# Optimization experiments

Measured on AMD Instinct MI355X. Metric: run time of the kernel, lower is better.

The kernel has to match this reference:

```python
import jax, jax.numpy as jnp
import numpy as np

N_NODES = 100000
N_EDGES = 1600000
NUM_FEATURES = 128
DIMS = [(NUM_FEATURES, 50), (50, 50), (50, 30), (30, 30), (30, 10), (10, 10), (10, 1)]


def setup_inputs() -> dict:
    key = jax.random.key(0)
    ks = jax.random.split(key, 4 + 2 * len(DIMS))
    inp = {
        "x": jax.random.normal(ks[0], (N_NODES, NUM_FEATURES), dtype=jnp.float32),
        "edge_index": jax.random.randint(ks[1], (2, N_EDGES), 0, N_NODES, dtype=jnp.int64) if jax.config.read("jax_enable_x64") else jax.random.randint(ks[1], (2, N_EDGES), 0, N_NODES, dtype=jnp.int32),
        "edge_weight": jax.random.uniform(ks[2], (N_EDGES,), dtype=jnp.float32),
    }
    for i, (fi, fo) in enumerate(DIMS):
        scale = 1.0 / np.sqrt(fi)
        inp[f"W{i+1}"] = jax.random.normal(ks[3 + 2 * i], (fi, fo), dtype=jnp.float32) * scale
        inp[f"b{i+1}"] = jax.random.normal(ks[4 + 2 * i], (fo,), dtype=jnp.float32) * 0.01
    return inp


def _gcn_norm(edge_index, edge_weight, n):
    # Add self-loops with weight 1, then symmetric normalization (PyG GCNConv).
    loops = jnp.arange(n)
    row = jnp.concatenate([edge_index[0], loops])
    col = jnp.concatenate([edge_index[1], loops])
    w = jnp.concatenate([edge_weight, jnp.ones((n,), edge_weight.dtype)])
    deg = jnp.zeros((n,), edge_weight.dtype).at[col].add(w)
    dinv = jnp.where(deg > 0, 1.0 / jnp.sqrt(deg), 0.0)
    norm = dinv[row] * w * dinv[col]
    return row, col, norm


def _gcn_conv(x, row, col, norm, W, b):
    h = x @ W                                # [N, out]
    msg = h[row] * norm[:, None]             # gather + edge scale [E+N, out]
    out = jnp.zeros_like(h).at[col].add(msg) # scatter-add
    return out + b


def _forward(x, edge_index, edge_weight, params):
    n = x.shape[0]
    row, col, norm = _gcn_norm(edge_index, edge_weight, n)  # shared across layers
    h = x
    n_layers = len(params)
    for i, (W, b) in enumerate(params):
        h = _gcn_conv(h, row, col, norm, W, b)
        if i < n_layers - 1:
            h = jax.nn.relu(h)
        # F.dropout treated as identity (eval mode) for a deterministic reference
    return h


def reference(x, edge_index, edge_weight, W1, b1, W2, b2, W3, b3, W4, b4, W5, b5, W6, b6, W7, b7):
    params = [(W1, b1), (W2, b2), (W3, b3), (W4, b4), (W5, b5), (W6, b6), (W7, b7)]
    return _forward(x, edge_index, edge_weight, params)
```

## Files before the change

### kernel.cpp

```cpp
#include <hip/hip_runtime.h>
#include <hip/hip_fp16.h>


static constexpr int NN = 100000;
static constexpr int NE = 1600000;
static constexpr int BKL = 9;
static constexpr int NBUK = (NN + 511) >> BKL;
static constexpr int EPT = 8;
static constexpr int EB = (NE + 2047) / 2048;


__global__ __launch_bounds__(256) void k_hist0(const int* __restrict__ col,
                                               int* __restrict__ counts) {
    __shared__ int lh[NBUK];
    for (int j = threadIdx.x; j < NBUK; j += 256) lh[j] = 0;
    __syncthreads();
    int base = blockIdx.x * 2048;
#pragma unroll
    for (int k = 0; k < EPT; ++k) {
        int e = base + k * 256 + threadIdx.x;
        if (e < NE) atomicAdd(&lh[col[e] >> BKL], 1);
    }
    __syncthreads();
    for (int j = threadIdx.x; j < NBUK; j += 256)
        counts[j * EB + blockIdx.x] = lh[j];
}


__global__ __launch_bounds__(256) void k_scanA(int* __restrict__ counts,
                                               int* __restrict__ btot) {
    __shared__ int lds[256];
    const int b = blockIdx.x;
    const int t = threadIdx.x;
    int* c = counts + (size_t)b * EB;
    constexpr int PER = (EB + 255) / 256;
    int v[PER];
    int s = 0;
#pragma unroll
    for (int k = 0; k < PER; ++k) {
        int idx = t * PER + k;
        v[k] = (idx < EB) ? c[idx] : 0;
        s += v[k];
    }
    lds[t] = s;
    __syncthreads();
    for (int off = 1; off < 256; off <<= 1) {
        int u = (t >= off) ? lds[t - off] : 0;
        __syncthreads();
        lds[t] += u;
        __syncthreads();
    }
    int run = lds[t] - s;
#pragma unroll
    for (int k = 0; k < PER; ++k) {
        int idx = t * PER + k;
        if (idx < EB) { c[idx] = run; run += v[k]; }
    }
    if (t == 255) btot[b] = lds[255];
}


__global__ void k_scanB(const int* __restrict__ btot, int* __restrict__ bstart) {
    __shared__ int lds[256];
    int t = threadIdx.x;
    int v = (t < NBUK) ? btot[t] : 0;
    lds[t] = v;
    __syncthreads();
    for (int off = 1; off < 256; off <<= 1) {
        int u = (t >= off) ? lds[t - off] : 0;
        __syncthreads();
        lds[t] += u;
        __syncthreads();
    }
    if (t < NBUK) bstart[t] = lds[t] - v;
    if (t == 0) bstart[NBUK] = NE;
}


__global__ __launch_bounds__(256) void k_A1(const int* __restrict__ row,
                                            const int* __restrict__ col,
                                            const float* __restrict__ ew,
                                            const int* __restrict__ counts,
                                            const int* __restrict__ bstart,
                                            int2* __restrict__ stg) {
    __shared__ int cur[NBUK];
    for (int j = threadIdx.x; j < NBUK; j += 256)
        cur[j] = bstart[j] + counts[j * EB + blockIdx.x];
    __syncthreads();
    int base = blockIdx.x * 2048;
#pragma unroll
    for (int k = 0; k < EPT; ++k) {
        int e = base + k * 256 + threadIdx.x;
        if (e < NE) {
            int c = col[e], r = row[e];
            int pos = atomicAdd(&cur[c >> BKL], 1);
            stg[pos] = make_int2(((c & 511) << 17) | r, __float_as_int(ew[e]));
        }
    }
}


__global__ __launch_bounds__(256) void k_bdeg(const int* __restrict__ bstart,
                                              const int2* __restrict__ stg,
                                              float* __restrict__ dinv) {
    __shared__ float sdeg[512];
    const int b = blockIdx.x;
    for (int j = threadIdx.x; j < 512; j += 256) sdeg[j] = 0.0f;
    __syncthreads();
    const int s = bstart[b], e = bstart[b + 1];
    for (int p = s + threadIdx.x; p < e; p += 256) {
        int2 rec = stg[p];
        atomicAdd(&sdeg[rec.x >> 17], __int_as_float(rec.y));
    }
    __syncthreads();
    for (int j = threadIdx.x; j < 512; j += 256) {
        int idx = (b << BKL) + j;
        if (idx < NN) dinv[idx] = rsqrtf(sdeg[j] + 1.0f);
    }
}


__global__ __launch_bounds__(512) void k_place(const int* __restrict__ bstart,
                                               const int2* __restrict__ stg,
                                               const float* __restrict__ dinv,
                                               int* __restrict__ offs,
                                               int2* __restrict__ csw) {
    __shared__ int lcnt[512];
    __shared__ int cur[512];
    const int b = blockIdx.x;
    const int t = threadIdx.x;
    lcnt[t] = 0;
    __syncthreads();
    const int s = bstart[b], e = bstart[b + 1];
    for (int p = s + t; p < e; p += 512)
        atomicAdd(&lcnt[stg[p].x >> 17], 1);
    __syncthreads();
    int v = lcnt[t];
    for (int off = 1; off < 512; off <<= 1) {
        int u = (t >= off) ? lcnt[t - off] : 0;
        __syncthreads();
        lcnt[t] += u;
        __syncthreads();
    }
    int excl = lcnt[t] - v;
    int idx = (b << BKL) + t;
    if (idx <= NN) offs[idx] = s + excl;
    cur[t] = s + excl;
    __syncthreads();
    for (int p = s + t; p < e; p += 512) {
        int2 rec = stg[p];
        int cl = rec.x >> 17;
        int r = rec.x & 0x1FFFF;
        float nw = dinv[r] * __int_as_float(rec.y) * dinv[(b << BKL) + cl];
        int slot = atomicAdd(&cur[cl], 1);
        csw[slot] = make_int2(r, __float_as_int(nw));
    }
}


template <int FIN, int FOUT, int S, int NSPL>
__global__ __launch_bounds__(256, 2) void k_matmul_f(const float* __restrict__ X,
                                                     const float* __restrict__ W,
                                                     __half* __restrict__ H) {
    constexpr int FC = FOUT / NSPL;
    constexpr int NG = FIN / 16;
    const int node = (blockIdx.x >> 1) * 256 + threadIdx.x;
    const int ch = blockIdx.x & 1;
    if (node >= NN) return;
    const float* xr = X + (size_t)node * FIN;
    float acc[FC];
#pragma unroll
    for (int j = 0; j < FC; ++j) acc[j] = 0.0f;

    float4 buf[2][4];
#pragma unroll
    for (int g = 0; g < 4; ++g) buf[0][g] = *(const float4*)(xr + 4 * g);
#pragma unroll
    for (int grp = 0; grp < NG; ++grp) {
        const int cur = grp & 1;
        if (grp + 1 < NG) {
#pragma unroll
            for (int g = 0; g < 4; ++g)
                buf[cur ^ 1][g] = *(const float4*)(xr + (grp + 1) * 16 + 4 * g);
        }
#pragma unroll
        for (int g = 0; g < 4; ++g)
#pragma unroll
            for (int kk = 0; kk < 4; ++kk) {
                float xv = ((const float*)&buf[cur][g])[kk];
                const float* wrow = W + (grp * 16 + 4 * g + kk) * FOUT + ch * FC;
#pragma unroll
                for (int j = 0; j < FC; ++j) acc[j] = fmaf(xv, wrow[j], acc[j]);
            }
    }
    __half* hr = H + (size_t)node * S + ch * FC;
#pragma unroll
    for (int j = 0; j < FC; ++j) hr[j] = __float2half_rn(acc[j]);
}


template <int FIN, int SX, int FOUT, int S, int NSPL>
__global__ __launch_bounds__(256, 2) void k_matmul_h(const __half* __restrict__ X,
                                                     const float* __restrict__ W,
                                                     __half* __restrict__ H) {
    constexpr int FC = FOUT / NSPL;
    constexpr int NCH = (FIN + 7) / 8;
    const int node = blockIdx.x * 256 + threadIdx.x;
    const int ch = blockIdx.y;
    if (node >= NN) return;
    const __half* xr = X + (size_t)node * SX;
    int4 raw[NCH];
#pragma unroll
    for (int c = 0; c < NCH; ++c) raw[c] = *(const int4*)(xr + 8 * c);
    float acc[FC];
#pragma unroll
    for (int j = 0; j < FC; ++j) acc[j] = 0.0f;
#pragma unroll
    for (int c = 0; c < NCH; ++c) {
        const __half2* hp = (const __half2*)&raw[c];
        const int lim = (FIN - 8 * c < 8) ? FIN - 8 * c : 8;
#pragma unroll
        for (int kk = 0; kk < 8; ++kk) {
            if (kk < lim) {
                __half2 pair = hp[kk >> 1];
                float xv = (kk & 1) ? __high2float(pair) : __low2float(pair);
                const float* wrow = W + (8 * c + kk) * FOUT + ch * FC;
#pragma unroll
                for (int j = 0; j < FC; ++j) acc[j] = fmaf(xv, wrow[j], acc[j]);
            }
        }
    }
    __half* hr = H + (size_t)node * S + ch * FC;
#pragma unroll
    for (int j = 0; j < FC; ++j) hr[j] = __float2half_rn(acc[j]);
}

__global__ void k_matmul_1h(const __half* __restrict__ X, const float* __restrict__ W,
                            float* __restrict__ H) {
    int i = blockIdx.x * blockDim.x + threadIdx.x;
    if (i >= NN) return;
    const __half* xr = X + (size_t)i * 16;
    int4 r0 = *(const int4*)xr;
    __half2 r1 = *(const __half2*)(xr + 8);
    const __half2* hp = (const __half2*)&r0;
    float acc = 0.0f;
#pragma unroll
    for (int q = 0; q < 4; ++q) {
        acc = fmaf(__low2float(hp[q]), W[2 * q], acc);
        acc = fmaf(__high2float(hp[q]), W[2 * q + 1], acc);
    }
    acc = fmaf(__low2float(r1), W[8], acc);
    acc = fmaf(__high2float(r1), W[9], acc);
    H[i] = acc;
}


static __device__ __forceinline__ int2 nt_load2(const int2* p) {
    unsigned long long raw = __builtin_nontemporal_load((const unsigned long long*)p);
    return make_int2((int)(raw & 0xFFFFFFFFull), (int)(raw >> 32));
}

template <int F, int SH, int SA, int LPN, bool RELU>
__global__ __launch_bounds__(256) void k_agg2(const int* __restrict__ offs,
                                              const int2* __restrict__ csw,
                                              const __half2* __restrict__ H,
                                              const float* __restrict__ dinv,
                                              const float* __restrict__ b,
                                              __half* __restrict__ O) {
    constexpr int R = F / 2;
    int t = blockIdx.x * blockDim.x + threadIdx.x;
    int g = t / LPN;
    int f = t - g * LPN;
    if (g >= NN) return;
    const int q0 = 4 * f;
    if (q0 >= R) return;
    int p = offs[g];
    const int pe = offs[g + 1];
    const int pl = pe - 1;

    float2 acc[4];
#pragma unroll
    for (int c = 0; c < 4; ++c) acc[c] = make_float2(0.f, 0.f);

    for (; p < pe; p += 4) {
        int2 e[4];
#pragma unroll
        for (int i = 0; i < 4; ++i) e[i] = nt_load2(csw + min(p + i, pl));
        __half2 h[4][4];
#pragma unroll
        for (int i = 0; i < 4; ++i)
            *(int4*)h[i] = *(const int4*)(H + (size_t)e[i].x * SH + q0);
#pragma unroll
        for (int i = 0; i < 4; ++i) {
            float w = (p + i < pe) ? __int_as_float(e[i].y) : 0.0f;
#pragma unroll
            for (int c = 0; c < 4; ++c) {
                acc[c].x = fmaf(__low2float(h[i][c]), w, acc[c].x);
                acc[c].y = fmaf(__high2float(h[i][c]), w, acc[c].y);
            }
        }
    }

    float di = dinv[g];
    float d2 = di * di;
    __half2 hs[4];
    *(int4*)hs = *(const int4*)(H + (size_t)g * SH + q0);
    __half2* orow = (__half2*)(O + (size_t)g * SA) + q0;
#pragma unroll
    for (int c = 0; c < 4; ++c) {
        if (q0 + c < R) {
            float vx = acc[c].x + fmaf(__low2float(hs[c]), d2, b[2 * (q0 + c)]);
            float vy = acc[c].y + fmaf(__high2float(hs[c]), d2, b[2 * (q0 + c) + 1]);
            if (RELU) { vx = fmaxf(vx, 0.f); vy = fmaxf(vy, 0.f); }
            orow[c] = __floats2half2_rn(vx, vy);
        }
    }
}

__global__ void k_agg1(const int* __restrict__ offs, const int2* __restrict__ csw,
                       const float* __restrict__ H, const float* __restrict__ dinv,
                       const float* __restrict__ b, float* __restrict__ O) {
    int g = blockIdx.x * blockDim.x + threadIdx.x;
    if (g >= NN) return;
    int p = offs[g];
    const int pe = offs[g + 1];
    const int pl = pe - 1;
    float a0 = 0.f, a1 = 0.f, a2 = 0.f, a3 = 0.f;
    for (; p < pe; p += 4) {
        int2 e0 = nt_load2(csw + min(p, pl)),     e1 = nt_load2(csw + min(p + 1, pl));
        int2 e2 = nt_load2(csw + min(p + 2, pl)), e3 = nt_load2(csw + min(p + 3, pl));
        float w0 = (p < pe)     ? __int_as_float(e0.y) : 0.f;
        float w1 = (p + 1 < pe) ? __int_as_float(e1.y) : 0.f;
        float w2 = (p + 2 < pe) ? __int_as_float(e2.y) : 0.f;
        float w3 = (p + 3 < pe) ? __int_as_float(e3.y) : 0.f;
        a0 = fmaf(H[e0.x], w0, a0);
        a1 = fmaf(H[e1.x], w1, a1);
        a2 = fmaf(H[e2.x], w2, a2);
        a3 = fmaf(H[e3.x], w3, a3);
    }
    float di = dinv[g];
    O[g] = ((a0 + a1) + (a2 + a3)) + fmaf(H[g], di * di, b[0]);
}


static inline size_t alignup(size_t x) { return (x + 255) & ~(size_t)255; }

extern "C" void kernel_launch(void* const* d_in, const int* in_sizes, int n_in,
                              void* d_out, int out_size, void* d_ws, size_t ws_size,
                              hipStream_t stream) {
    const float* x  = (const float*)d_in[0];
    const int*   ei = (const int*)d_in[1];
    const float* ew = (const float*)d_in[2];
    const float* Wp[7];
    const float* Bp[7];
    for (int l = 0; l < 7; ++l) {
        Wp[l] = (const float*)d_in[3 + 2 * l];
        Bp[l] = (const float*)d_in[4 + 2 * l];
    }
    const int* row = ei;
    const int* col = ei + NE;

    char* ws = (char*)d_ws;
    float* dinv  = (float*)ws;  ws += alignup((size_t)NN * 4);
    char*  Hb    = ws;          ws += alignup((size_t)NN * 64 * 2);
    char*  Aa    = ws;          ws += alignup((size_t)NN * 64 * 2);
    char*  Ab    = ws;          ws += alignup((size_t)NN * 64 * 2);
    int*   offs  = (int*)ws;    ws += alignup((size_t)(NN + 1) * 4);
    int*   counts= (int*)ws;    ws += alignup((size_t)NBUK * EB * 4);
    int*   btot  = (int*)ws;    ws += alignup((size_t)NBUK * 4);
    int*   bstart= (int*)ws;    ws += alignup((size_t)(NBUK + 1) * 4);
    int2*  stg   = (int2*)ws;   ws += alignup((size_t)NE * 8);
    int2*  csw   = (int2*)ws;   ws += alignup((size_t)NE * 8);

    const int gN = (NN + 255) / 256;

    k_hist0<<<EB, 256, 0, stream>>>(col, counts);
    k_scanA<<<NBUK, 256, 0, stream>>>(counts, btot);
    k_scanB<<<1, 256, 0, stream>>>(btot, bstart);
    k_A1<<<EB, 256, 0, stream>>>(row, col, ew, counts, bstart, stg);
    k_bdeg<<<NBUK, 256, 0, stream>>>(bstart, stg, dinv);
    k_place<<<NBUK, 512, 0, stream>>>(bstart, stg, dinv, offs, csw);

#define AGG(FOUT, S, LPN, RELU, OUT, LIDX)                                                  \
    k_agg2<FOUT, (S) / 2, S, LPN, RELU>                                                     \
        <<<((size_t)NN * (LPN) + 255) / 256, 256, 0, stream>>>(                             \
            offs, csw, (const __half2*)Hb, dinv, Bp[LIDX], (__half*)(OUT))

    k_matmul_f<128, 50, 64, 2><<<gN * 2, 256, 0, stream>>>(x, Wp[0], (__half*)Hb);
    AGG(50, 64, 8, true, Aa, 0);
    k_matmul_h<50, 64, 50, 64, 2><<<dim3(gN, 2), 256, 0, stream>>>((const __half*)Aa, Wp[1], (__half*)Hb);
    AGG(50, 64, 8, true, Ab, 1);
    k_matmul_h<50, 64, 30, 32, 2><<<dim3(gN, 2), 256, 0, stream>>>((const __half*)Ab, Wp[2], (__half*)Hb);
    AGG(30, 32, 4, true, Aa, 2);
    k_matmul_h<30, 32, 30, 32, 2><<<dim3(gN, 2), 256, 0, stream>>>((const __half*)Aa, Wp[3], (__half*)Hb);
    AGG(30, 32, 4, true, Ab, 3);
    k_matmul_h<30, 32, 10, 16, 1><<<dim3(gN, 1), 256, 0, stream>>>((const __half*)Ab, Wp[4], (__half*)Hb);
    AGG(10, 16, 2, true, Aa, 4);
    k_matmul_h<10, 16, 10, 16, 1><<<dim3(gN, 1), 256, 0, stream>>>((const __half*)Aa, Wp[5], (__half*)Hb);
    AGG(10, 16, 2, true, Ab, 5);
#undef AGG

    k_matmul_1h<<<gN, 256, 0, stream>>>((const __half*)Ab, Wp[6], (float*)Hb);
    k_agg1<<<gN, 256, 0, stream>>>(offs, csw, (const float*)Hb, dinv, Bp[6],
                                   (float*)d_out);
}
```

Before: 482.5 us.

## Use split-bf16 MFMA for first-layer 128x50 matmul

Replaces the per-thread scalar FMA first-layer matmul with a 64-row tile kernel. Each X and W element is split into high and low bf16 parts, staged in swizzled LDS, and multiplied with three 16x16x32 bf16 MFMA passes to approximate fp32 accuracy. The goal is to remove the FMA-bound, uncoalesced per-node row reads and redundant W loads of the old kernel. In exchange it adds the conversion work, recomputes the W split in every block, uses 64KB of LDS per block, and drops the low*low term, which costs a little precision.

```diff
diff --git a/kernel.cpp b/kernel.cpp
--- a/kernel.cpp
+++ b/kernel.cpp
@@ -158,45 +158,118 @@
 }
 
 
-template <int FIN, int FOUT, int S, int NSPL>
-__global__ __launch_bounds__(256, 2) void k_matmul_f(const float* __restrict__ X,
-                                                     const float* __restrict__ W,
-                                                     __half* __restrict__ H) {
-    constexpr int FC = FOUT / NSPL;
-    constexpr int NG = FIN / 16;
-    const int node = (blockIdx.x >> 1) * 256 + threadIdx.x;
-    const int ch = blockIdx.x & 1;
-    if (node >= NN) return;
-    const float* xr = X + (size_t)node * FIN;
-    float acc[FC];
-#pragma unroll
-    for (int j = 0; j < FC; ++j) acc[j] = 0.0f;
-
-    float4 buf[2][4];
-#pragma unroll
-    for (int g = 0; g < 4; ++g) buf[0][g] = *(const float4*)(xr + 4 * g);
-#pragma unroll
-    for (int grp = 0; grp < NG; ++grp) {
-        const int cur = grp & 1;
-        if (grp + 1 < NG) {
-#pragma unroll
-            for (int g = 0; g < 4; ++g)
-                buf[cur ^ 1][g] = *(const float4*)(xr + (grp + 1) * 16 + 4 * g);
-        }
-#pragma unroll
-        for (int g = 0; g < 4; ++g)
-#pragma unroll
-            for (int kk = 0; kk < 4; ++kk) {
-                float xv = ((const float*)&buf[cur][g])[kk];
-                const float* wrow = W + (grp * 16 + 4 * g + kk) * FOUT + ch * FC;
-#pragma unroll
-                for (int j = 0; j < FC; ++j) acc[j] = fmaf(xv, wrow[j], acc[j]);
+typedef short s16x8 __attribute__((ext_vector_type(8)));
+typedef short s16x4 __attribute__((ext_vector_type(4)));
+typedef short s16x2 __attribute__((ext_vector_type(2)));
+typedef float f32x4v __attribute__((ext_vector_type(4)));
+
+static __device__ __forceinline__ unsigned short bf16rn(float f) {
+    unsigned u = __float_as_uint(f);
+    return (unsigned short)((u + 0x7FFFu + ((u >> 16) & 1u)) >> 16);
+}
+
+#define SWZ(r, k) ((k) ^ (((r) & 7) << 3))
+
+__global__ __launch_bounds__(256) void k_matmul_f(const float* __restrict__ X,
+                                                  const float* __restrict__ W,
+                                                  __half* __restrict__ H) {
+    __shared__ short lds[4 * 64 * 128];
+    constexpr int XH = 0, XL = 8192, WHo = 16384, WLo = 24576;
+    const int t = threadIdx.x;
+    const int blk = blockIdx.x;
+
+    {
+        const int g = t & 31;
+        const int rs = t >> 5;
+#pragma unroll
+        for (int i = 0; i < 8; ++i) {
+            const int r = rs + 8 * i;
+            const int row = blk * 64 + r;
+            float4 v = make_float4(0.f, 0.f, 0.f, 0.f);
+            if (row < NN) v = *(const float4*)(X + (size_t)row * 128 + g * 4);
+            const float* vf = (const float*)&v;
+            short h[4], l[4];
+#pragma unroll
+            for (int e = 0; e < 4; ++e) {
+                unsigned short hb = bf16rn(vf[e]);
+                float hf = __uint_as_float((unsigned)hb << 16);
+                h[e] = (short)hb;
+                l[e] = (short)bf16rn(vf[e] - hf);
             }
-    }
-    __half* hr = H + (size_t)node * S + ch * FC;
-#pragma unroll
-    for (int j = 0; j < FC; ++j) hr[j] = __float2half_rn(acc[j]);
-}
+            const int k0 = SWZ(r, 4 * g);
+            *(s16x4*)&lds[XH + r * 128 + k0] = *(const s16x4*)h;
+            *(s16x4*)&lds[XL + r * 128 + k0] = *(const s16x4*)l;
+        }
+    }
+    {
+        const int c = t & 63;
+        const int kq = t >> 6;
+#pragma unroll
+        for (int i = 0; i < 32; i += 2) {
+            const int k = kq * 32 + i;
+            float w0 = 0.f, w1 = 0.f;
+            if (c < 50) { w0 = W[k * 50 + c]; w1 = W[(k + 1) * 50 + c]; }
+            unsigned short h0 = bf16rn(w0), h1 = bf16rn(w1);
+            float f0 = __uint_as_float((unsigned)h0 << 16);
+            float f1 = __uint_as_float((unsigned)h1 << 16);
+            short hh[2] = {(short)h0, (short)h1};
+            short ll[2] = {(short)bf16rn(w0 - f0), (short)bf16rn(w1 - f1)};
+            const int k0 = SWZ(c, k);
+            *(s16x2*)&lds[WHo + c * 128 + k0] = *(const s16x2*)hh;
+            *(s16x2*)&lds[WLo + c * 128 + k0] = *(const s16x2*)ll;
+        }
+    }
+    __syncthreads();
+
+    const int w = t >> 6;
+    const int lane = t & 63;
+    const int lr = lane & 15;
+    const int kg = lane >> 4;
+    const int ar = 16 * w + lr;
+    f32x4v acc[4];
+#pragma unroll
+    for (int ct = 0; ct < 4; ++ct) acc[ct] = (f32x4v){0.f, 0.f, 0.f, 0.f};
+
+#pragma unroll
+    for (int kb = 0; kb < 4; ++kb) {
+        const int kf = kb * 32 + kg * 8;
+        const int ka = SWZ(ar, kf);
+        s16x8 ah = *(const s16x8*)&lds[XH + ar * 128 + ka];
+        s16x8 al = *(const s16x8*)&lds[XL + ar * 128 + ka];
+        s16x8 bh[4], bl[4];
+#pragma unroll
+        for (int ct = 0; ct < 4; ++ct) {
+            const int bc = ct * 16 + lr;
+            const int kbo = SWZ(bc, kf);
+            bh[ct] = *(const s16x8*)&lds[WHo + bc * 128 + kbo];
+            bl[ct] = *(const s16x8*)&lds[WLo + bc * 128 + kbo];
+        }
+#pragma unroll
+        for (int ct = 0; ct < 4; ++ct)
+            acc[ct] = __builtin_amdgcn_mfma_f32_16x16x32_bf16(ah, bh[ct], acc[ct], 0, 0, 0);
+#pragma unroll
+        for (int ct = 0; ct < 4; ++ct)
+            acc[ct] = __builtin_amdgcn_mfma_f32_16x16x32_bf16(ah, bl[ct], acc[ct], 0, 0, 0);
+#pragma unroll
+        for (int ct = 0; ct < 4; ++ct)
+            acc[ct] = __builtin_amdgcn_mfma_f32_16x16x32_bf16(al, bh[ct], acc[ct], 0, 0, 0);
+    }
+
+    const int gr = blk * 64 + 16 * w + kg * 4;
+#pragma unroll
+    for (int ct = 0; ct < 4; ++ct) {
+        const int col = ct * 16 + lr;
+        if (col < 50) {
+#pragma unroll
+            for (int rg = 0; rg < 4; ++rg) {
+                const int row = gr + rg;
+                if (row < NN)
+                    H[(size_t)row * 64 + col] = __float2half_rn(acc[ct][rg]);
+            }
+        }
+    }
+}
+#undef SWZ
 
 
 template <int FIN, int SX, int FOUT, int S, int NSPL>
@@ -373,6 +446,7 @@
     int2*  csw   = (int2*)ws;   ws += alignup((size_t)NE * 8);
 
     const int gN = (NN + 255) / 256;
+    const int gM = (NN + 63) / 64;
 
     k_hist0<<<EB, 256, 0, stream>>>(col, counts);
     k_scanA<<<NBUK, 256, 0, stream>>>(counts, btot);
@@ -386,7 +460,7 @@
         <<<((size_t)NN * (LPN) + 255) / 256, 256, 0, stream>>>(                             \
             offs, csw, (const __half2*)Hb, dinv, Bp[LIDX], (__half*)(OUT))
 
-    k_matmul_f<128, 50, 64, 2><<<gN * 2, 256, 0, stream>>>(x, Wp[0], (__half*)Hb);
+    k_matmul_f<<<gM, 256, 0, stream>>>(x, Wp[0], (__half*)Hb);
     AGG(50, 64, 8, true, Aa, 0);
     k_matmul_h<50, 64, 50, 64, 2><<<dim3(gN, 2), 256, 0, stream>>>((const __half*)Aa, Wp[1], (__half*)Hb);
     AGG(50, 64, 8, true, Ab, 1);
```

New measurement: 479.9 us. No clear change (-0.5%).
